# Optimization experiments

Measured on AMD Instinct MI355X. Metric: run time of the kernel, lower is better.

Reference implementation:

```python
import jax, jax.numpy as jnp
import numpy as np

D_MODEL = 1024
N_HEADS = 16
HEAD_DIM = D_MODEL // N_HEADS
NEG_INF = -1e9


def setup_inputs() -> dict:
    key = jax.random.key(0)
    ks = jax.random.split(key, 12)
    B, S = 2, 2048
    std = 1.0 / np.sqrt(D_MODEL)
    def lin(k):
        kw, kb = jax.random.split(k)
        W = jax.random.uniform(kw, (D_MODEL, D_MODEL), jnp.float32, -std, std)
        b = jax.random.uniform(kb, (D_MODEL,), jnp.float32, -std, std)
        return W, b
    Wq, bq = lin(ks[0])
    Wk, bk = lin(ks[1])
    Wv, bv = lin(ks[2])
    Wo, bo = lin(ks[3])
    Q = jax.random.normal(ks[4], (B, S, D_MODEL), jnp.float32)
    K = jax.random.normal(ks[5], (B, S, D_MODEL), jnp.float32)
    V = jax.random.normal(ks[6], (B, S, D_MODEL), jnp.float32)
    # causal attention mask: True means masked (disallowed)
    attn_mask = jnp.triu(jnp.ones((S, S), dtype=bool), k=1)
    padding_mask = jnp.zeros((B, S), dtype=bool)  # no padding
    return {"Q": Q, "K": K, "V": V, "attn_mask": attn_mask,
            "padding_mask": padding_mask,
            "Wq": Wq, "bq": bq, "Wk": Wk, "bk": bk,
            "Wv": Wv, "bv": bv, "Wo": Wo, "bo": bo}


def reference(Q, K, V, attn_mask, padding_mask, Wq, bq, Wk, bk, Wv, bv, Wo, bo):
    B, Sq, _ = Q.shape
    Sk = K.shape[1]
    # QKV projections, split into heads -> [B, H, S, Dh]
    def proj(x, W, b):
        y = x @ W.T + b
        return y.reshape(B, -1, N_HEADS, HEAD_DIM).transpose(0, 2, 1, 3)
    q = proj(Q, Wq, bq)
    k = proj(K, Wk, bk)
    v = proj(V, Wv, bv)
    # scaled dot-product attention (dropout is identity in eval mode)
    scores = jnp.einsum('bhqd,bhkd->bhqk', q, k) / jnp.sqrt(
        jnp.asarray(HEAD_DIM, q.dtype))
    mask = attn_mask[None, None, :, :] | padding_mask[:, None, None, :]
    scores = jnp.where(mask, NEG_INF, scores)
    attn = jax.nn.softmax(scores, axis=-1)
    x = jnp.einsum('bhqk,bhkd->bhqd', attn, v)
    x = x.transpose(0, 2, 1, 3).reshape(B, Sq, D_MODEL)
    return x @ Wo.T + bo
```

## Files before the change

### kernel.cpp

```cpp
#include <hip/hip_runtime.h>
#include <hip/hip_bf16.h>
#include <cstddef>
#include <cstdint>

#define S_LEN  2048
#define DMODEL 1024
#define NHEADS 16

typedef __attribute__((ext_vector_type(8))) short  short8;
typedef __attribute__((ext_vector_type(4))) short  s16x4;
typedef __attribute__((ext_vector_type(8))) __bf16 bf16x8;
typedef __attribute__((ext_vector_type(4))) float  f32x4;

__device__ __forceinline__ f32x4 MFMA(short8 a, short8 b, f32x4 c) {
    return __builtin_amdgcn_mfma_f32_16x16x32_bf16(
        __builtin_bit_cast(bf16x8, a), __builtin_bit_cast(bf16x8, b), c, 0, 0, 0);
}

__device__ __forceinline__ unsigned short f2bs(float f) {
    return __builtin_bit_cast(unsigned short, __float2bfloat16(f));
}
__device__ __forceinline__ float bs2f(unsigned short u) {
    unsigned int x = ((unsigned int)u) << 16;
    return __builtin_bit_cast(float, x);
}

__device__ __forceinline__ short8 cvt8(f32x4 a, f32x4 b) {
    short8 r;
#pragma unroll
    for (int i = 0; i < 4; ++i) {
        r[i]     = (short)f2bs(a[i]);
        r[4 + i] = (short)f2bs(b[i]);
    }
    return r;
}

__device__ __forceinline__ short8 scale8(short8 v) {
    short8 r;
#pragma unroll
    for (int i = 0; i < 8; ++i)
        r[i] = (short)f2bs(bs2f((unsigned short)v[i]) * 0.125f);
    return r;
}

__device__ __forceinline__ int xcd_swz(int bid, int nwg) {
    const int chunk = nwg >> 3;
    return (bid & 7) * chunk + (bid >> 3);
}

__device__ __forceinline__ void bar_sync() {
    asm volatile("s_waitcnt lgkmcnt(0)" ::: "memory");
    __builtin_amdgcn_sched_barrier(0);
    __builtin_amdgcn_s_barrier();
}

#define GLDS16(src, dst) __builtin_amdgcn_global_load_lds( \
    (__attribute__((address_space(1))) void*)(src),        \
    (__attribute__((address_space(3))) void*)(dst), 16, 0, 0)

__global__ __launch_bounds__(256)
void wcvt(const float* __restrict__ Wq, const float* __restrict__ Wk,
          const float* __restrict__ Wv, unsigned short* __restrict__ wb)
{
    const int i = blockIdx.x * 256 + threadIdx.x;
    const float* src = (i < 131072) ? Wq : (i < 262144) ? Wk : Wv;
    const size_t j = (size_t)(i & 131071) * 8;
    const short8 v = cvt8(((const f32x4*)(src + j))[0], ((const f32x4*)(src + j))[1]);
    *(short8*)(wb + (size_t)i * 8) = v;
}

struct FS { f32x4 v[2][2]; };

template<bool A_F32>
__device__ __forceinline__ void gemm_body(const void* __restrict__ Ap,
                                          const void* __restrict__ Wp,
                                          const float* __restrict__ bias,
                                          void* __restrict__ outp,
                                          int m0, int n0)
{
    __shared__ short a_lds[2][128 * 32];
    __shared__ short w_lds[2][128 * 32];
    const int t    = threadIdx.x;
    const int lane = t & 63;
    const int wid  = t >> 6;
    const int wr   = (wid >> 1) << 6;
    const int wc   = (wid & 1) << 6;
    const int fr   = lane & 15;
    const int ks   = lane >> 4;

    const int row0 = t >> 2,         sl0 = t & 3;
    const int row1 = (256 + t) >> 2, sl1 = (256 + t) & 3;
    const int ms0  = sl0 ^ ((row0 >> 1) & 3);
    const int ms1  = sl1 ^ ((row1 >> 1) & 3);

    const int g0 = wid * 2, g1 = g0 + 1;
    const int gsl   = lane & 3;
    const int grow0 = g0 * 16 + (lane >> 2);
    const int grow1 = g1 * 16 + (lane >> 2);
    const int ssl0  = gsl ^ ((grow0 >> 1) & 3);
    const int ssl1  = gsl ^ ((grow1 >> 1) & 3);

    const float* Rp             = (const float*)(A_F32 ? Ap : Wp);
    const unsigned short* Gp    = (const unsigned short*)(A_F32 ? Wp : Ap);
    const int rbase             = A_F32 ? m0 : n0;
    const int gbase             = A_F32 ? n0 : m0;
    short (*r_lds)[128 * 32]    = A_F32 ? a_lds : w_lds;
    short (*g_lds)[128 * 32]    = A_F32 ? w_lds : a_lds;

    auto load_R = [&](FS& S, int k0) {
        const float* p0 = Rp + (size_t)(rbase + row0) * DMODEL + k0 + sl0 * 8;
        S.v[0][0] = ((const f32x4*)p0)[0]; S.v[0][1] = ((const f32x4*)p0)[1];
        const float* p1 = Rp + (size_t)(rbase + row1) * DMODEL + k0 + sl1 * 8;
        S.v[1][0] = ((const f32x4*)p1)[0]; S.v[1][1] = ((const f32x4*)p1)[1];
    };
    auto store_R = [&](const FS& S, int buf) {
        *(short8*)&r_lds[buf][row0 * 32 + ms0 * 8] = cvt8(S.v[0][0], S.v[0][1]);
        *(short8*)&r_lds[buf][row1 * 32 + ms1 * 8] = cvt8(S.v[1][0], S.v[1][1]);
    };
    auto gload_G = [&](int k0, int buf) {
        GLDS16(Gp + (size_t)(gbase + grow0) * DMODEL + k0 + ssl0 * 8,
               &g_lds[buf][g0 * 512]);
        GLDS16(Gp + (size_t)(gbase + grow1) * DMODEL + k0 + ssl1 * 8,
               &g_lds[buf][g1 * 512]);
    };

    f32x4 acc[4][4] = {};

    auto compute = [&](int cur) {
        short8 af[4], bfr[4];
#pragma unroll
        for (int i = 0; i < 4; ++i) {
            const int ra = wr + i * 16 + fr;
            af[i]  = *(const short8*)&a_lds[cur][ra * 32 + ((ks ^ ((ra >> 1) & 3)) << 3)];
            const int rb = wc + i * 16 + fr;
            bfr[i] = *(const short8*)&w_lds[cur][rb * 32 + ((ks ^ ((rb >> 1) & 3)) << 3)];
        }
#pragma unroll
        for (int mi = 0; mi < 4; ++mi)
#pragma unroll
            for (int ni = 0; ni < 4; ++ni)
                acc[mi][ni] = MFMA(af[mi], bfr[ni], acc[mi][ni]);
    };

    FS SA, SB;
    gload_G(0, 0);
    load_R(SA, 0);
    store_R(SA, 0);
    load_R(SB, 32);
    bar_sync();

    for (int tt = 0; tt < 30; tt += 2) {
        gload_G((tt + 1) * 32, 1);
        load_R(SA, (tt + 2) * 32);
        compute(0);
        store_R(SB, 1);
        asm volatile("s_waitcnt vmcnt(4)" ::: "memory");
        bar_sync();
        gload_G((tt + 2) * 32, 0);
        load_R(SB, (tt + 3) * 32);
        compute(1);
        store_R(SA, 0);
        asm volatile("s_waitcnt vmcnt(4)" ::: "memory");
        bar_sync();
    }
    gload_G(31 * 32, 1);
    compute(0);
    store_R(SB, 1);
    asm volatile("s_waitcnt vmcnt(0)" ::: "memory");
    bar_sync();
    compute(1);

#pragma unroll
    for (int ni = 0; ni < 4; ++ni) {
        const int n    = n0 + wc + ni * 16 + fr;
        const float bv = bias[n];
#pragma unroll
        for (int mi = 0; mi < 4; ++mi) {
#pragma unroll
            for (int j = 0; j < 4; ++j) {
                const int m = m0 + wr + mi * 16 + ks * 4 + j;
                const float val = acc[mi][ni][j] + bv;
                if constexpr (A_F32) {
                    const int b = m >> 11, s = m & (S_LEN - 1);
                    const int hh = n >> 6, dh = n & 63;
                    ((unsigned short*)outp)[((((size_t)b * NHEADS + hh) * S_LEN + s) << 6) + dh]
                        = f2bs(val);
                } else {
                    ((float*)outp)[(size_t)m * DMODEL + n] = val;
                }
            }
        }
    }
}

__global__ __launch_bounds__(256, 3)
void qkv_gemm(const float* __restrict__ Q, const float* __restrict__ K,
              const float* __restrict__ V,
              const unsigned short* __restrict__ wb,
              const float* __restrict__ bq, const float* __restrict__ bk,
              const float* __restrict__ bv,
              unsigned short* qh, unsigned short* kh, unsigned short* vh)
{
    const int swz = xcd_swz(blockIdx.x, 768);
    const int z   = swz >> 8;
    const int rem = swz & 255;
    const int my  = rem >> 3;
    const int nx  = rem & 7;
    const float *A, *B; unsigned short* O;
    if (z == 0)      { A = Q; B = bq; O = qh; }
    else if (z == 1) { A = K; B = bk; O = kh; }
    else             { A = V; B = bv; O = vh; }
    gemm_body<true>(A, wb + ((size_t)z << 20), B, O, my * 128, nx * 128);
}

__global__ __launch_bounds__(256, 3)
void out_gemm(const unsigned short* __restrict__ X, const float* __restrict__ Wo,
              const float* __restrict__ bo, float* __restrict__ out)
{
    const int swz = xcd_swz(blockIdx.x, 256);
    gemm_body<false>(X, Wo, bo, out, (swz >> 3) * 128, (swz & 7) * 128);
}

#define VSTR 72
#define PSTR 88

struct QState {
    short8 qf0, qf1;
    f32x4  oacc[4];
    float  m, l;
    int    qr0;
};

__device__ __forceinline__ void attn_tile(QState& st, const int k0,
                                          const short* k_lds, const short* v_lds,
                                          short* p_buf, const int fr, const int ks)
{
    const int myq = st.qr0 + fr;
    f32x4 sacc[4] = {};
    __builtin_amdgcn_s_setprio(1);
#pragma unroll
    for (int nk = 0; nk < 4; ++nk) {
        const int rb = nk * 16 + fr;
        short8 a0 = *(const short8*)&k_lds[rb * 64 + (((ks)     ^ (rb & 7)) << 3)];
        short8 a1 = *(const short8*)&k_lds[rb * 64 + (((4 + ks) ^ (rb & 7)) << 3)];
        sacc[nk] = MFMA(a0, st.qf0, sacc[nk]);
        sacc[nk] = MFMA(a1, st.qf1, sacc[nk]);
    }
    __builtin_amdgcn_s_setprio(0);

    float mx = -1e9f;
    if (k0 + 63 <= st.qr0) {
#pragma unroll
        for (int nk = 0; nk < 4; ++nk)
#pragma unroll
            for (int jj = 0; jj < 4; ++jj) mx = fmaxf(mx, sacc[nk][jj]);
    } else {
#pragma unroll
        for (int nk = 0; nk < 4; ++nk)
#pragma unroll
            for (int jj = 0; jj < 4; ++jj) {
                const int key = k0 + nk * 16 + ks * 4 + jj;
                float s = (key <= myq) ? sacc[nk][jj] : -1e9f;
                sacc[nk][jj] = s;
                mx = fmaxf(mx, s);
            }
    }
    mx = fmaxf(mx, __shfl_xor(mx, 16));
    mx = fmaxf(mx, __shfl_xor(mx, 32));
    if (!__all(mx <= st.m + 8.f)) {
        const float mnew = fmaxf(st.m, mx);
        const float corr = __expf(st.m - mnew);
        st.m = mnew;
        st.l *= corr;
#pragma unroll
        for (int nd = 0; nd < 4; ++nd)
#pragma unroll
            for (int jj = 0; jj < 4; ++jj) st.oacc[nd][jj] *= corr;
    }

    float rsum = 0.f;
#pragma unroll
    for (int nk = 0; nk < 4; ++nk) {
        s16x4 pw;
#pragma unroll
        for (int jj = 0; jj < 4; ++jj) {
            const float p = __expf(sacc[nk][jj] - st.m);
            rsum += p;
            pw[jj] = (short)f2bs(p);
        }
        *(s16x4*)&p_buf[fr * PSTR + nk * 16 + ks * 4] = pw;
    }
    rsum += __shfl_xor(rsum, 16);
    rsum += __shfl_xor(rsum, 32);
    st.l += rsum;
    asm volatile("" ::: "memory");

    __builtin_amdgcn_s_setprio(1);
#pragma unroll
    for (int sh = 0; sh < 2; ++sh) {
        short8 pa = *(const short8*)&p_buf[fr * PSTR + sh * 32 + ks * 8];
#pragma unroll
        for (int nd = 0; nd < 4; ++nd) {
            short8 vf = *(const short8*)&v_lds[(nd * 16 + fr) * VSTR + sh * 32 + ks * 8];
            st.oacc[nd] = MFMA(vf, pa, st.oacc[nd]);
        }
    }
    __builtin_amdgcn_s_setprio(0);
}

__global__ __launch_bounds__(256, 2)
void attn_kernel(const unsigned short* __restrict__ qh,
                 const unsigned short* __restrict__ kh,
                 const unsigned short* __restrict__ vh,
                 unsigned short* __restrict__ xh)
{
    __shared__ short k_lds[64 * 64];
    __shared__ short v_lds[64 * VSTR];
    __shared__ short p_lds[4][16 * PSTR];

    const int t    = threadIdx.x;
    const int lane = t & 63;
    const int wid  = t >> 6;
    const int fr   = lane & 15;
    const int ks   = lane >> 4;
    const int swz  = xcd_swz(blockIdx.x, 512);
    const int bh   = swz >> 4;
    const int xp   = swz & 15;
    const int qa0  = xp * 64;
    const int qb0  = (31 - xp) * 64;
    const int ntA  = xp + 1;
    const int ntB  = 32 - xp;

    const unsigned short* qb_ = qh + ((size_t)bh << 17);
    const unsigned short* kb  = kh + ((size_t)bh << 17);
    const unsigned short* vb  = vh + ((size_t)bh << 17);

    QState A, B;
    A.qr0 = qa0 + wid * 16;  B.qr0 = qb0 + wid * 16;
    A.qf0 = scale8(*(const short8*)&qb_[(A.qr0 + fr) * 64 + ks * 8]);
    A.qf1 = scale8(*(const short8*)&qb_[(A.qr0 + fr) * 64 + 32 + ks * 8]);
    B.qf0 = scale8(*(const short8*)&qb_[(B.qr0 + fr) * 64 + ks * 8]);
    B.qf1 = scale8(*(const short8*)&qb_[(B.qr0 + fr) * 64 + 32 + ks * 8]);
#pragma unroll
    for (int nd = 0; nd < 4; ++nd) { A.oacc[nd] = f32x4{}; B.oacc[nd] = f32x4{}; }
    A.m = B.m = -1e9f; A.l = B.l = 0.f;

    short8 kv[2], vv[2];
#pragma unroll
    for (int cc = 0; cc < 2; ++cc) {
        const int c   = cc * 256 + t;
        const int row = c >> 3;
        const int sl  = c & 7;
        kv[cc] = *(const short8*)(kb + (size_t)row * 64 + sl * 8);
        const int key = c & 63;
        const int d0  = (c >> 6) * 8;
        vv[cc] = *(const short8*)(vb + (size_t)key * 64 + d0);
    }

    for (int kt = 0; kt < ntB; ++kt) {
        const int k0 = kt * 64;
        bar_sync();

#pragma unroll
        for (int cc = 0; cc < 2; ++cc) {
            const int c   = cc * 256 + t;
            const int row = c >> 3;
            const int ms  = (c & 7) ^ (row & 7);
            *(short8*)&k_lds[row * 64 + ms * 8] = kv[cc];
            const int key = c & 63;
            const int d0  = (c >> 6) * 8;
#pragma unroll
            for (int i = 0; i < 8; ++i)
                v_lds[(d0 + i) * VSTR + key] = vv[cc][i];
        }
        bar_sync();

        if (kt + 1 < ntB) {
            const int k1 = k0 + 64;
#pragma unroll
            for (int cc = 0; cc < 2; ++cc) {
                const int c   = cc * 256 + t;
                const int row = c >> 3;
                const int sl  = c & 7;
                kv[cc] = *(const short8*)(kb + (size_t)(k1 + row) * 64 + sl * 8);
                const int key = c & 63;
                const int d0  = (c >> 6) * 8;
                vv[cc] = *(const short8*)(vb + (size_t)(k1 + key) * 64 + d0);
            }
        }

        attn_tile(B, k0, k_lds, v_lds, p_lds[wid], fr, ks);
        if (kt < ntA)
            attn_tile(A, k0, k_lds, v_lds, p_lds[wid], fr, ks);
    }

    const int b = bh >> 4, h = bh & 15;
#pragma unroll
    for (int which = 0; which < 2; ++which) {
        QState& st = which ? B : A;
        const float inv = 1.f / st.l;
        const size_t base = ((size_t)b * S_LEN + (st.qr0 + fr)) * DMODEL + h * 64;
#pragma unroll
        for (int nd = 0; nd < 4; ++nd)
#pragma unroll
            for (int jj = 0; jj < 4; ++jj)
                xh[base + nd * 16 + ks * 4 + jj] = f2bs(st.oacc[nd][jj] * inv);
    }
}

extern "C" void kernel_launch(void* const* d_in, const int* in_sizes, int n_in,
                              void* d_out, int out_size, void* d_ws, size_t ws_size,
                              hipStream_t stream)
{
    const float* Q  = (const float*)d_in[0];
    const float* K  = (const float*)d_in[1];
    const float* V  = (const float*)d_in[2];
    const float* Wq = (const float*)d_in[5];
    const float* bq = (const float*)d_in[6];
    const float* Wk = (const float*)d_in[7];
    const float* bk = (const float*)d_in[8];
    const float* Wv = (const float*)d_in[9];
    const float* bv = (const float*)d_in[10];
    const float* Wo = (const float*)d_in[11];
    const float* bo = (const float*)d_in[12];
    float* out = (float*)d_out;

    const size_t HSZ = (size_t)2 * S_LEN * DMODEL;
    unsigned short* qh = (unsigned short*)d_ws;
    unsigned short* kh = qh + HSZ;
    unsigned short* vh = kh + HSZ;
    unsigned short* xh = vh + HSZ;
    unsigned short* wb = xh;

    wcvt<<<1536, 256, 0, stream>>>(Wq, Wk, Wv, wb);
    qkv_gemm<<<768, 256, 0, stream>>>(Q, K, V, wb, bq, bk, bv, qh, kh, vh);
    attn_kernel<<<512, 256, 0, stream>>>(qh, kh, vh, xh);
    out_gemm<<<256, 256, 0, stream>>>(xh, Wo, bo, out);
}
```

Measured before the change: 118.9 us.

## Rewrite QKV projection GEMM with 256x256 tiles, 8 waves and phased MFMA scheduling

The fused QKV projection GEMM becomes a dedicated kernel using 256x256 output tiles, a K-step of 64 and 512 threads per block. Global loads, LDS writes and MFMA groups are interleaved across four barrier-separated phases, with s_setprio raised around the MFMA bursts. The goal is more data reuse per tile and better overlap of fp32-to-bf16 conversion and loads with matrix math. The cost is only 192 blocks for a 256-CU device and a large LDS footprint (about 128KB), so some CUs sit idle and occupancy is one block per CU. The out-projection GEMM is specialised from the old shared template with no change in behaviour.

```diff
diff --git a/kernel.cpp b/kernel.cpp
--- a/kernel.cpp
+++ b/kernel.cpp
@@ -52,6 +52,12 @@
     asm volatile("s_waitcnt lgkmcnt(0)" ::: "memory");
     __builtin_amdgcn_sched_barrier(0);
     __builtin_amdgcn_s_barrier();
+}
+
+__device__ __forceinline__ void phase_sync() {
+    __builtin_amdgcn_s_barrier();
+    asm volatile("s_waitcnt lgkmcnt(0)" ::: "memory");
+    __builtin_amdgcn_sched_barrier(0);
 }
 
 #define GLDS16(src, dst) __builtin_amdgcn_global_load_lds( \
@@ -69,17 +75,157 @@
     *(short8*)(wb + (size_t)i * 8) = v;
 }
 
+__global__ __launch_bounds__(512, 2)
+void qkv_gemm(const float* __restrict__ Q, const float* __restrict__ K,
+              const float* __restrict__ V,
+              const unsigned short* __restrict__ wb,
+              const float* __restrict__ bq, const float* __restrict__ bk,
+              const float* __restrict__ bv,
+              unsigned short* qh, unsigned short* kh, unsigned short* vh)
+{
+    __shared__ short a_lds[2][256 * 64];
+    __shared__ short w_lds[2][256 * 64];
+
+    const int swz = xcd_swz(blockIdx.x, 192);
+    const int z   = swz >> 6;
+    const int rem = swz & 63;
+    const int m0  = (rem >> 2) * 256;
+    const int n0  = (rem & 3) * 256;
+
+    const float* A; const float* bias_; unsigned short* O;
+    if (z == 0)      { A = Q; bias_ = bq; O = qh; }
+    else if (z == 1) { A = K; bias_ = bk; O = kh; }
+    else             { A = V; bias_ = bv; O = vh; }
+    const unsigned short* W = wb + ((size_t)z << 20);
+
+    const int t    = threadIdx.x;
+    const int lane = t & 63;
+    const int wid  = t >> 6;
+    const int wm   = wid >> 2;
+    const int wn   = wid & 3;
+    const int fr   = lane & 15;
+    const int ks   = lane >> 4;
+
+    f32x4 La[4][2];
+
+    auto aload = [&](int k0, int cc) {
+        const int c   = cc * 512 + t;
+        const int row = c >> 3, sl = c & 7;
+        const float* p = A + (size_t)(m0 + row) * DMODEL + k0 + sl * 8;
+        La[cc][0] = ((const f32x4*)p)[0];
+        La[cc][1] = ((const f32x4*)p)[1];
+    };
+    auto awrite = [&](int cc, int buf) {
+        const int c   = cc * 512 + t;
+        const int row = c >> 3, sl = c & 7;
+        *(short8*)&a_lds[buf][row * 64 + (sl ^ (row & 7)) * 8]
+            = cvt8(La[cc][0], La[cc][1]);
+    };
+    auto wload = [&](int k0, int j, int buf) {
+        const int r = (wid * 4 + j) * 8 + (lane >> 3);
+        const int srccol = ((lane & 7) ^ (r & 7)) * 8;
+        GLDS16(W + (size_t)(n0 + r) * DMODEL + k0 + srccol,
+               &w_lds[buf][(wid * 4 + j) * 512]);
+    };
+
+    short8 af[4], bfr[4];
+    auto read_b = [&](int buf, int kk) {
+#pragma unroll
+        for (int ni = 0; ni < 4; ++ni) {
+            const int row = wn * 64 + ni * 16 + fr;
+            bfr[ni] = *(const short8*)&w_lds[buf][row * 64 + (((kk * 4 + ks) ^ (row & 7)) << 3)];
+        }
+    };
+    auto read_a = [&](int buf, int kk, int rbase) {
+#pragma unroll
+        for (int i = 0; i < 4; ++i) {
+            const int row = rbase + i * 16 + fr;
+            af[i] = *(const short8*)&a_lds[buf][row * 64 + (((kk * 4 + ks) ^ (row & 7)) << 3)];
+        }
+    };
+
+    f32x4 acc0[4][4] = {}, acc1[4][4] = {};
+    auto mfma16 = [&](f32x4 (&acc)[4][4]) {
+        __builtin_amdgcn_s_setprio(1);
+#pragma unroll
+        for (int i = 0; i < 4; ++i)
+#pragma unroll
+            for (int ni = 0; ni < 4; ++ni)
+                acc[i][ni] = MFMA(af[i], bfr[ni], acc[i][ni]);
+        __builtin_amdgcn_s_setprio(0);
+    };
+
+    wload(0, 0, 0); wload(0, 1, 0); wload(0, 2, 0); wload(0, 3, 0);
+    aload(0, 0); aload(0, 1); aload(0, 2); aload(0, 3);
+    awrite(0, 0); awrite(1, 0); awrite(2, 0); awrite(3, 0);
+    asm volatile("s_waitcnt vmcnt(0)" ::: "memory");
+    bar_sync();
+
+    const int rb0 = wm * 128, rb1 = wm * 128 + 64;
+
+    for (int tk = 0; tk < 16; ++tk) {
+        const int c  = tk & 1;
+        const int nb = c ^ 1;
+        const int k1 = (tk + 1) * 64;
+        const bool st = tk < 15;
+
+        if (st) { wload(k1, 0, nb); aload(k1, 0); aload(k1, 1); }
+        read_b(c, 0); read_a(c, 0, rb0);
+        phase_sync();
+        mfma16(acc0);
+        __builtin_amdgcn_s_barrier();
+        if (st) { wload(k1, 1, nb); aload(k1, 2); aload(k1, 3); }
+        read_a(c, 0, rb1);
+        phase_sync();
+        mfma16(acc1);
+        __builtin_amdgcn_s_barrier();
+        if (st) { wload(k1, 2, nb); awrite(0, nb); awrite(1, nb); }
+        read_b(c, 1); read_a(c, 1, rb0);
+        phase_sync();
+        mfma16(acc0);
+        __builtin_amdgcn_s_barrier();
+        if (st) { wload(k1, 3, nb); awrite(2, nb); awrite(3, nb); }
+        read_a(c, 1, rb1);
+        phase_sync();
+        mfma16(acc1);
+        if (st) asm volatile("s_waitcnt vmcnt(0)" ::: "memory");
+        __builtin_amdgcn_s_barrier();
+    }
+
+    auto epi = [&](f32x4 (&acc)[4][4], int mbase) {
+#pragma unroll
+        for (int ni = 0; ni < 4; ++ni) {
+            const int n    = n0 + wn * 64 + ni * 16 + fr;
+            const float bv = bias_[n];
+#pragma unroll
+            for (int i = 0; i < 4; ++i) {
+#pragma unroll
+                for (int j = 0; j < 4; ++j) {
+                    const int m = m0 + mbase + i * 16 + ks * 4 + j;
+                    const int b = m >> 11, s = m & (S_LEN - 1);
+                    const int hh = n >> 6, dh = n & 63;
+                    O[((((size_t)b * NHEADS + hh) * S_LEN + s) << 6) + dh]
+                        = f2bs(acc[i][ni][j] + bv);
+                }
+            }
+        }
+    };
+    epi(acc0, wm * 128);
+    epi(acc1, wm * 128 + 64);
+}
+
 struct FS { f32x4 v[2][2]; };
 
-template<bool A_F32>
-__device__ __forceinline__ void gemm_body(const void* __restrict__ Ap,
-                                          const void* __restrict__ Wp,
-                                          const float* __restrict__ bias,
-                                          void* __restrict__ outp,
-                                          int m0, int n0)
+__global__ __launch_bounds__(256, 3)
+void out_gemm(const unsigned short* __restrict__ X, const float* __restrict__ Wo,
+              const float* __restrict__ bo, float* __restrict__ out)
 {
     __shared__ short a_lds[2][128 * 32];
     __shared__ short w_lds[2][128 * 32];
+    const int swz = xcd_swz(blockIdx.x, 256);
+    const int m0  = (swz >> 3) * 128;
+    const int n0  = (swz & 7) * 128;
+
     const int t    = threadIdx.x;
     const int lane = t & 63;
     const int wid  = t >> 6;
@@ -100,32 +246,22 @@
     const int ssl0  = gsl ^ ((grow0 >> 1) & 3);
     const int ssl1  = gsl ^ ((grow1 >> 1) & 3);
 
-    const float* Rp             = (const float*)(A_F32 ? Ap : Wp);
-    const unsigned short* Gp    = (const unsigned short*)(A_F32 ? Wp : Ap);
-    const int rbase             = A_F32 ? m0 : n0;
-    const int gbase             = A_F32 ? n0 : m0;
-    short (*r_lds)[128 * 32]    = A_F32 ? a_lds : w_lds;
-    short (*g_lds)[128 * 32]    = A_F32 ? w_lds : a_lds;
-
     auto load_R = [&](FS& S, int k0) {
-        const float* p0 = Rp + (size_t)(rbase + row0) * DMODEL + k0 + sl0 * 8;
+        const float* p0 = Wo + (size_t)(n0 + row0) * DMODEL + k0 + sl0 * 8;
         S.v[0][0] = ((const f32x4*)p0)[0]; S.v[0][1] = ((const f32x4*)p0)[1];
-        const float* p1 = Rp + (size_t)(rbase + row1) * DMODEL + k0 + sl1 * 8;
+        const float* p1 = Wo + (size_t)(n0 + row1) * DMODEL + k0 + sl1 * 8;
         S.v[1][0] = ((const f32x4*)p1)[0]; S.v[1][1] = ((const f32x4*)p1)[1];
     };
     auto store_R = [&](const FS& S, int buf) {
-        *(short8*)&r_lds[buf][row0 * 32 + ms0 * 8] = cvt8(S.v[0][0], S.v[0][1]);
-        *(short8*)&r_lds[buf][row1 * 32 + ms1 * 8] = cvt8(S.v[1][0], S.v[1][1]);
+        *(short8*)&w_lds[buf][row0 * 32 + ms0 * 8] = cvt8(S.v[0][0], S.v[0][1]);
+        *(short8*)&w_lds[buf][row1 * 32 + ms1 * 8] = cvt8(S.v[1][0], S.v[1][1]);
     };
     auto gload_G = [&](int k0, int buf) {
-        GLDS16(Gp + (size_t)(gbase + grow0) * DMODEL + k0 + ssl0 * 8,
-               &g_lds[buf][g0 * 512]);
-        GLDS16(Gp + (size_t)(gbase + grow1) * DMODEL + k0 + ssl1 * 8,
-               &g_lds[buf][g1 * 512]);
+        GLDS16(X + (size_t)(m0 + grow0) * DMODEL + k0 + ssl0 * 8, &a_lds[buf][g0 * 512]);
+        GLDS16(X + (size_t)(m0 + grow1) * DMODEL + k0 + ssl1 * 8, &a_lds[buf][g1 * 512]);
     };
 
     f32x4 acc[4][4] = {};
-
     auto compute = [&](int cur) {
         short8 af[4], bfr[4];
 #pragma unroll
@@ -173,52 +309,15 @@
 #pragma unroll
     for (int ni = 0; ni < 4; ++ni) {
         const int n    = n0 + wc + ni * 16 + fr;
-        const float bv = bias[n];
-#pragma unroll
-        for (int mi = 0; mi < 4; ++mi) {
+        const float bv = bo[n];
+#pragma unroll
+        for (int mi = 0; mi < 4; ++mi)
 #pragma unroll
             for (int j = 0; j < 4; ++j) {
                 const int m = m0 + wr + mi * 16 + ks * 4 + j;
-                const float val = acc[mi][ni][j] + bv;
-                if constexpr (A_F32) {
-                    const int b = m >> 11, s = m & (S_LEN - 1);
-                    const int hh = n >> 6, dh = n & 63;
-                    ((unsigned short*)outp)[((((size_t)b * NHEADS + hh) * S_LEN + s) << 6) + dh]
-                        = f2bs(val);
-                } else {
-                    ((float*)outp)[(size_t)m * DMODEL + n] = val;
-                }
+                out[(size_t)m * DMODEL + n] = acc[mi][ni][j] + bv;
             }
-        }
-    }
-}
-
-__global__ __launch_bounds__(256, 3)
-void qkv_gemm(const float* __restrict__ Q, const float* __restrict__ K,
-              const float* __restrict__ V,
-              const unsigned short* __restrict__ wb,
-              const float* __restrict__ bq, const float* __restrict__ bk,
-              const float* __restrict__ bv,
-              unsigned short* qh, unsigned short* kh, unsigned short* vh)
-{
-    const int swz = xcd_swz(blockIdx.x, 768);
-    const int z   = swz >> 8;
-    const int rem = swz & 255;
-    const int my  = rem >> 3;
-    const int nx  = rem & 7;
-    const float *A, *B; unsigned short* O;
-    if (z == 0)      { A = Q; B = bq; O = qh; }
-    else if (z == 1) { A = K; B = bk; O = kh; }
-    else             { A = V; B = bv; O = vh; }
-    gemm_body<true>(A, wb + ((size_t)z << 20), B, O, my * 128, nx * 128);
-}
-
-__global__ __launch_bounds__(256, 3)
-void out_gemm(const unsigned short* __restrict__ X, const float* __restrict__ Wo,
-              const float* __restrict__ bo, float* __restrict__ out)
-{
-    const int swz = xcd_swz(blockIdx.x, 256);
-    gemm_body<false>(X, Wo, bo, out, (swz >> 3) * 128, (swz & 7) * 128);
+    }
 }
 
 #define VSTR 72
@@ -433,7 +532,7 @@
     unsigned short* wb = xh;
 
     wcvt<<<1536, 256, 0, stream>>>(Wq, Wk, Wv, wb);
-    qkv_gemm<<<768, 256, 0, stream>>>(Q, K, V, wb, bq, bk, bv, qh, kh, vh);
+    qkv_gemm<<<192, 512, 0, stream>>>(Q, K, V, wb, bq, bk, bv, qh, kh, vh);
     attn_kernel<<<512, 256, 0, stream>>>(qh, kh, vh, xh);
     out_gemm<<<256, 256, 0, stream>>>(xh, Wo, bo, out);
 }
```

After: 130.4 us. 1.1x slower.

## Split shared GEMM body and simplify out-projection pipeline to register-staged loads

Applied to the files above, without the earlier changes.

Removes the templated gemm_body and inlines it into qkv_gemm and out_gemm. The out projection drops direct global-to-LDS loads for the bf16 activations and uses a simpler double-buffered loop: register-staged loads with one __syncthreads per k step. The attention kernel's custom barrier (explicit lgkmcnt wait plus sched_barrier) is replaced with __syncthreads. This simplifies scheduling but may lose the deeper prefetch and finer wait control of the old pipeline.

```diff
diff --git a/kernel.cpp b/kernel.cpp
--- a/kernel.cpp
+++ b/kernel.cpp
@@ -57,6 +57,8 @@
 #define GLDS16(src, dst) __builtin_amdgcn_global_load_lds( \
     (__attribute__((address_space(1))) void*)(src),        \
     (__attribute__((address_space(3))) void*)(dst), 16, 0, 0)
+
+struct FS { f32x4 v[2][2]; };
 
 __global__ __launch_bounds__(256)
 void wcvt(const float* __restrict__ Wq, const float* __restrict__ Wk,
@@ -69,17 +71,29 @@
     *(short8*)(wb + (size_t)i * 8) = v;
 }
 
-struct FS { f32x4 v[2][2]; };
-
-template<bool A_F32>
-__device__ __forceinline__ void gemm_body(const void* __restrict__ Ap,
-                                          const void* __restrict__ Wp,
-                                          const float* __restrict__ bias,
-                                          void* __restrict__ outp,
-                                          int m0, int n0)
+__global__ __launch_bounds__(256, 3)
+void qkv_gemm(const float* __restrict__ Q, const float* __restrict__ K,
+              const float* __restrict__ V,
+              const unsigned short* __restrict__ wb,
+              const float* __restrict__ bq, const float* __restrict__ bk,
+              const float* __restrict__ bv,
+              unsigned short* qh, unsigned short* kh, unsigned short* vh)
 {
     __shared__ short a_lds[2][128 * 32];
     __shared__ short w_lds[2][128 * 32];
+
+    const int swz = xcd_swz(blockIdx.x, 768);
+    const int z   = swz >> 8;
+    const int rem = swz & 255;
+    const int m0  = (rem >> 3) * 128;
+    const int n0  = (rem & 7) * 128;
+
+    const float *A, *B_; unsigned short* O;
+    if (z == 0)      { A = Q; B_ = bq; O = qh; }
+    else if (z == 1) { A = K; B_ = bk; O = kh; }
+    else             { A = V; B_ = bv; O = vh; }
+    const unsigned short* W = wb + ((size_t)z << 20);
+
     const int t    = threadIdx.x;
     const int lane = t & 63;
     const int wid  = t >> 6;
@@ -100,32 +114,22 @@
     const int ssl0  = gsl ^ ((grow0 >> 1) & 3);
     const int ssl1  = gsl ^ ((grow1 >> 1) & 3);
 
-    const float* Rp             = (const float*)(A_F32 ? Ap : Wp);
-    const unsigned short* Gp    = (const unsigned short*)(A_F32 ? Wp : Ap);
-    const int rbase             = A_F32 ? m0 : n0;
-    const int gbase             = A_F32 ? n0 : m0;
-    short (*r_lds)[128 * 32]    = A_F32 ? a_lds : w_lds;
-    short (*g_lds)[128 * 32]    = A_F32 ? w_lds : a_lds;
-
     auto load_R = [&](FS& S, int k0) {
-        const float* p0 = Rp + (size_t)(rbase + row0) * DMODEL + k0 + sl0 * 8;
+        const float* p0 = A + (size_t)(m0 + row0) * DMODEL + k0 + sl0 * 8;
         S.v[0][0] = ((const f32x4*)p0)[0]; S.v[0][1] = ((const f32x4*)p0)[1];
-        const float* p1 = Rp + (size_t)(rbase + row1) * DMODEL + k0 + sl1 * 8;
+        const float* p1 = A + (size_t)(m0 + row1) * DMODEL + k0 + sl1 * 8;
         S.v[1][0] = ((const f32x4*)p1)[0]; S.v[1][1] = ((const f32x4*)p1)[1];
     };
     auto store_R = [&](const FS& S, int buf) {
-        *(short8*)&r_lds[buf][row0 * 32 + ms0 * 8] = cvt8(S.v[0][0], S.v[0][1]);
-        *(short8*)&r_lds[buf][row1 * 32 + ms1 * 8] = cvt8(S.v[1][0], S.v[1][1]);
+        *(short8*)&a_lds[buf][row0 * 32 + ms0 * 8] = cvt8(S.v[0][0], S.v[0][1]);
+        *(short8*)&a_lds[buf][row1 * 32 + ms1 * 8] = cvt8(S.v[1][0], S.v[1][1]);
     };
     auto gload_G = [&](int k0, int buf) {
-        GLDS16(Gp + (size_t)(gbase + grow0) * DMODEL + k0 + ssl0 * 8,
-               &g_lds[buf][g0 * 512]);
-        GLDS16(Gp + (size_t)(gbase + grow1) * DMODEL + k0 + ssl1 * 8,
-               &g_lds[buf][g1 * 512]);
+        GLDS16(W + (size_t)(n0 + grow0) * DMODEL + k0 + ssl0 * 8, &w_lds[buf][g0 * 512]);
+        GLDS16(W + (size_t)(n0 + grow1) * DMODEL + k0 + ssl1 * 8, &w_lds[buf][g1 * 512]);
     };
 
     f32x4 acc[4][4] = {};
-
     auto compute = [&](int cur) {
         short8 af[4], bfr[4];
 #pragma unroll
@@ -173,52 +177,104 @@
 #pragma unroll
     for (int ni = 0; ni < 4; ++ni) {
         const int n    = n0 + wc + ni * 16 + fr;
-        const float bv = bias[n];
+        const float bv = B_[n];
 #pragma unroll
         for (int mi = 0; mi < 4; ++mi) {
 #pragma unroll
             for (int j = 0; j < 4; ++j) {
                 const int m = m0 + wr + mi * 16 + ks * 4 + j;
-                const float val = acc[mi][ni][j] + bv;
-                if constexpr (A_F32) {
-                    const int b = m >> 11, s = m & (S_LEN - 1);
-                    const int hh = n >> 6, dh = n & 63;
-                    ((unsigned short*)outp)[((((size_t)b * NHEADS + hh) * S_LEN + s) << 6) + dh]
-                        = f2bs(val);
-                } else {
-                    ((float*)outp)[(size_t)m * DMODEL + n] = val;
-                }
+                const int b = m >> 11, s = m & (S_LEN - 1);
+                const int hh = n >> 6, dh = n & 63;
+                O[((((size_t)b * NHEADS + hh) * S_LEN + s) << 6) + dh]
+                    = f2bs(acc[mi][ni][j] + bv);
             }
         }
     }
-}
-
-__global__ __launch_bounds__(256, 3)
-void qkv_gemm(const float* __restrict__ Q, const float* __restrict__ K,
-              const float* __restrict__ V,
-              const unsigned short* __restrict__ wb,
-              const float* __restrict__ bq, const float* __restrict__ bk,
-              const float* __restrict__ bv,
-              unsigned short* qh, unsigned short* kh, unsigned short* vh)
-{
-    const int swz = xcd_swz(blockIdx.x, 768);
-    const int z   = swz >> 8;
-    const int rem = swz & 255;
-    const int my  = rem >> 3;
-    const int nx  = rem & 7;
-    const float *A, *B; unsigned short* O;
-    if (z == 0)      { A = Q; B = bq; O = qh; }
-    else if (z == 1) { A = K; B = bk; O = kh; }
-    else             { A = V; B = bv; O = vh; }
-    gemm_body<true>(A, wb + ((size_t)z << 20), B, O, my * 128, nx * 128);
 }
 
 __global__ __launch_bounds__(256, 3)
 void out_gemm(const unsigned short* __restrict__ X, const float* __restrict__ Wo,
               const float* __restrict__ bo, float* __restrict__ out)
 {
+    __shared__ short a_lds[2][128 * 32];
+    __shared__ short w_lds[2][128 * 32];
     const int swz = xcd_swz(blockIdx.x, 256);
-    gemm_body<false>(X, Wo, bo, out, (swz >> 3) * 128, (swz & 7) * 128);
+    const int m0  = (swz >> 3) * 128;
+    const int n0  = (swz & 7) * 128;
+
+    const int t    = threadIdx.x;
+    const int lane = t & 63;
+    const int wid  = t >> 6;
+    const int wr   = (wid >> 1) << 6;
+    const int wc   = (wid & 1) << 6;
+    const int fr   = lane & 15;
+    const int ks   = lane >> 4;
+
+    const int row0 = t >> 2,         sl0 = t & 3;
+    const int row1 = (256 + t) >> 2, sl1 = (256 + t) & 3;
+    const int ms0  = sl0 ^ ((row0 >> 1) & 3);
+    const int ms1  = sl1 ^ ((row1 >> 1) & 3);
+
+    short8 av_b[2];
+    f32x4  wv_f[2][2];
+
+    auto load_tile = [&](int k0) {
+        av_b[0] = *(const short8*)(X + (size_t)(m0 + row0) * DMODEL + k0 + sl0 * 8);
+        av_b[1] = *(const short8*)(X + (size_t)(m0 + row1) * DMODEL + k0 + sl1 * 8);
+        const float* pw0 = Wo + (size_t)(n0 + row0) * DMODEL + k0 + sl0 * 8;
+        wv_f[0][0] = ((const f32x4*)pw0)[0]; wv_f[0][1] = ((const f32x4*)pw0)[1];
+        const float* pw1 = Wo + (size_t)(n0 + row1) * DMODEL + k0 + sl1 * 8;
+        wv_f[1][0] = ((const f32x4*)pw1)[0]; wv_f[1][1] = ((const f32x4*)pw1)[1];
+    };
+    auto store_tile = [&](int buf) {
+        *(short8*)&a_lds[buf][row0 * 32 + ms0 * 8] = av_b[0];
+        *(short8*)&a_lds[buf][row1 * 32 + ms1 * 8] = av_b[1];
+        *(short8*)&w_lds[buf][row0 * 32 + ms0 * 8] = cvt8(wv_f[0][0], wv_f[0][1]);
+        *(short8*)&w_lds[buf][row1 * 32 + ms1 * 8] = cvt8(wv_f[1][0], wv_f[1][1]);
+    };
+
+    load_tile(0);
+    store_tile(0);
+    load_tile(32);
+    __syncthreads();
+
+    f32x4 acc[4][4] = {};
+
+    for (int kidx = 0; kidx < 32; ++kidx) {
+        const int cur = kidx & 1;
+        short8 af[4], bfr[4];
+#pragma unroll
+        for (int i = 0; i < 4; ++i) {
+            const int ra = wr + i * 16 + fr;
+            af[i]  = *(const short8*)&a_lds[cur][ra * 32 + ((ks ^ ((ra >> 1) & 3)) << 3)];
+            const int rb = wc + i * 16 + fr;
+            bfr[i] = *(const short8*)&w_lds[cur][rb * 32 + ((ks ^ ((rb >> 1) & 3)) << 3)];
+        }
+#pragma unroll
+        for (int mi = 0; mi < 4; ++mi)
+#pragma unroll
+            for (int ni = 0; ni < 4; ++ni)
+                acc[mi][ni] = MFMA(af[mi], bfr[ni], acc[mi][ni]);
+
+        if (kidx + 1 < 32) {
+            store_tile(cur ^ 1);
+            if (kidx + 2 < 32) load_tile((kidx + 2) * 32);
+        }
+        __syncthreads();
+    }
+
+#pragma unroll
+    for (int ni = 0; ni < 4; ++ni) {
+        const int n    = n0 + wc + ni * 16 + fr;
+        const float bv = bo[n];
+#pragma unroll
+        for (int mi = 0; mi < 4; ++mi)
+#pragma unroll
+            for (int j = 0; j < 4; ++j) {
+                const int m = m0 + wr + mi * 16 + ks * 4 + j;
+                out[(size_t)m * DMODEL + n] = acc[mi][ni][j] + bv;
+            }
+    }
 }
 
 #define VSTR 72
@@ -359,7 +415,7 @@
 
     for (int kt = 0; kt < ntB; ++kt) {
         const int k0 = kt * 64;
-        bar_sync();
+        __syncthreads();
 
 #pragma unroll
         for (int cc = 0; cc < 2; ++cc) {
@@ -373,7 +429,7 @@
             for (int i = 0; i < 8; ++i)
                 v_lds[(d0 + i) * VSTR + key] = vv[cc][i];
         }
-        bar_sync();
+        __syncthreads();
 
         if (kt + 1 < ntB) {
             const int k1 = k0 + 64;
```

Measured after the change: 109.1 us. 1.09x faster.
